# Optimization experiments

Hardware: AMD Instinct MI355X
Metric: run time of the kernel (lower is better)

The kernel has to match this reference:

```python
import jax, jax.numpy as jnp
import numpy as np

DIM = 192
HEADS = 6
HEAD_DIM = DIM // HEADS
K = 3          # kernel_size
PAD = 1
STRIDE = 2
SCALE = HEAD_DIM ** -0.5
B, H, W = 16, 56, 56


def setup_inputs() -> dict:
    key = jax.random.key(0)
    ks = jax.random.split(key, 6)
    x = jax.random.normal(ks[0], (B, H, W, DIM), jnp.float32)
    # Linear weights stored as [in, out] so y = x @ W + b (== torch x @ W.T)
    Wv = jax.random.normal(ks[1], (DIM, DIM), jnp.float32) * 0.05          # v_pj, no bias
    Wa = jax.random.normal(ks[2], (DIM, K**4 * HEADS), jnp.float32) * 0.05  # attn linear
    ba = jax.random.normal(ks[3], (K**4 * HEADS,), jnp.float32) * 0.01
    Wp = jax.random.normal(ks[4], (DIM, DIM), jnp.float32) * 0.05           # proj
    bp = jax.random.normal(ks[5], (DIM,), jnp.float32) * 0.01
    return {"x": x, "Wv": Wv, "Wa": Wa, "ba": ba, "Wp": Wp, "bp": bp}


def reference(x, Wv, Wa, ba, Wp, bp):
    # Dropout layers act as identity (eval mode).
    Bn, Hn, Wn, C = x.shape
    h = -(-Hn // STRIDE)  # ceil(H/stride) = 28
    w = -(-Wn // STRIDE)
    KK = K * K

    # --- value projection + unfold (im2col over K x K window, stride STRIDE) ---
    v = x @ Wv  # [B,H,W,C]
    vp = jnp.pad(v, ((0, 0), (PAD, PAD), (PAD, PAD), (0, 0)))
    # patches: [B,h,w,K*K,C]; loop is over the fixed 3x3 kernel taps only
    patches = jnp.stack(
        [vp[:, i:i + STRIDE * h:STRIDE, j:j + STRIDE * w:STRIDE, :]
         for i in range(K) for j in range(K)], axis=3)
    patches = patches.reshape(Bn, h * w, KK, HEADS, HEAD_DIM)

    # --- attention weights from avg-pooled map (H divisible by STRIDE here) ---
    pooled = x.reshape(Bn, h, STRIDE, w, STRIDE, C).mean(axis=(2, 4))  # [B,h,w,C]
    a = pooled.reshape(Bn, h * w, C) @ Wa + ba                         # [B,hw,K^4*heads]
    a = a.reshape(Bn, h * w, HEADS, KK, KK) * SCALE
    a = jax.nn.softmax(a, axis=-1)

    # --- windowed attention: [B,hw,heads,K2,K2] x [B,hw,K2,heads,hd] ---
    out = jnp.einsum('bnhpq,bnqhd->bnphd', a, patches)  # [B,hw,K2,heads,hd]
    out = out.reshape(Bn, h, w, KK, C)

    # --- fold (scatter-add of overlapping patches back to HxW) ---
    acc = jnp.zeros((Bn, Hn + 2 * PAD, Wn + 2 * PAD, C), x.dtype)
    idx = 0
    for i in range(K):
        for j in range(K):
            acc = acc.at[:, i:i + STRIDE * h:STRIDE, j:j + STRIDE * w:STRIDE, :].add(out[:, :, :, idx, :])
            idx += 1
    y = acc[:, PAD:PAD + Hn, PAD:PAD + Wn, :]

    return y @ Wp + bp
```

## Files before the change

kernel.cpp:

```cpp
#include <hip/hip_runtime.h>
#include <cstdint>
#include <cstddef>

#define DIMC    192
#define NHEADS  6
#define NATT    486
#define NB      16
#define NH      56
#define NWW     56
#define HPOOL   28
#define WPOOL   28
#define NPIX    784
#define VH      58
#define VW      58
#define MROWS   (NB*NH*NWW)
#define MPOOL   (NB*NPIX)
#define SCALE_A 0.17677669529663687f

using bf16x8 = __attribute__((ext_vector_type(8))) short;
using f32x4  = __attribute__((ext_vector_type(4))) float;

static __device__ __forceinline__ unsigned short f2bf(float f) {
    unsigned int u = __float_as_uint(f);
    unsigned int r = (u + 0x7fffu + ((u >> 16) & 1u)) >> 16;
    return (unsigned short)r;
}
static __device__ __forceinline__ float bf2f(unsigned short u) {
    return __uint_as_float((unsigned int)u << 16);
}

__global__ __launch_bounds__(256)
void prep_kernel(const float* __restrict__ Wv, const float* __restrict__ Wp,
                 const float* __restrict__ Wa,
                 unsigned short* __restrict__ WTv, unsigned short* __restrict__ WTp,
                 unsigned short* __restrict__ WaT, unsigned int* __restrict__ vpu)
{
    int idx = blockIdx.x * 256 + threadIdx.x;
    if (idx < 73728) {
        int sel = idx / 36864;
        int r   = idx - sel * 36864;
        int n   = r / DIMC;
        int k   = r - n * DIMC;
        const float* W = sel ? Wp : Wv;
        unsigned short* WT = sel ? WTp : WTv;
        WT[r] = f2bf(W[k * DIMC + n]);
    } else if (idx < 172032) {
        int r = idx - 73728;
        int n = r / DIMC;
        int k = r - n * DIMC;
        WaT[r] = (n < NATT) ? f2bf(Wa[(size_t)k * NATT + n] * SCALE_A) : (unsigned short)0;
    } else {
        int i2   = idx - 172032;
        int cu   = i2 % 96;
        int rest = i2 / 96;
        int b    = rest / 228;
        int p    = rest - b * 228;
        int hi, wi;
        if (p < 58)       { hi = 0;  wi = p; }
        else if (p < 116) { hi = 57; wi = p - 58; }
        else { int q = p - 116; hi = 1 + (q >> 1); wi = (q & 1) * 57; }
        vpu[(((size_t)b * VH + hi) * VW + wi) * 96 + cu] = 0u;
    }
}

static __device__ __forceinline__
void gemm0_body(const float* __restrict__ x, const unsigned short* __restrict__ WT,
                unsigned short* __restrict__ vp, int by, int t, char* smem)
{
    unsigned short* As = (unsigned short*)smem;

    const int l  = t & 63;
    const int w  = t >> 6;
    const int wr = w >> 1;
    const int wc = w & 1;

    const float* Ab = x + (size_t)by * 128 * DIMC;
#pragma unroll
    for (int i = 0; i < 12; ++i) {
        int f = i * 2048 + t * 4;
        float4 v = *(const float4*)(Ab + f);
        int row = f / DIMC;
        int k   = f - row * DIMC;
        ushort4 u;
        u.x = f2bf(v.x); u.y = f2bf(v.y); u.z = f2bf(v.z); u.w = f2bf(v.w);
        int off = (row * 384 + k * 2) ^ ((row & 7) << 4);
        *(ushort4*)((char*)As + off) = u;
    }
    __syncthreads();

    f32x4 acc[2][6];
#pragma unroll
    for (int mi = 0; mi < 2; ++mi)
#pragma unroll
        for (int ni = 0; ni < 6; ++ni) acc[mi][ni] = (f32x4)0.f;

    const int arow0 = wr * 32 + (l & 15);
    const int kb    = (l >> 4) << 4;

#pragma unroll
    for (int ks = 0; ks < 6; ++ks) {
        bf16x8 a[2], b[6];
#pragma unroll
        for (int mi = 0; mi < 2; ++mi) {
            int row = arow0 + mi * 16;
            int off = (row * 384 + ks * 64 + kb) ^ ((row & 7) << 4);
            a[mi] = *(const bf16x8*)((const char*)As + off);
        }
#pragma unroll
        for (int ni = 0; ni < 6; ++ni) {
            int n = wc * 96 + ni * 16 + (l & 15);
            b[ni] = *(const bf16x8*)(WT + (size_t)n * DIMC + ks * 32 + ((l >> 4) << 3));
        }
#pragma unroll
        for (int mi = 0; mi < 2; ++mi)
#pragma unroll
            for (int ni = 0; ni < 6; ++ni)
                acc[mi][ni] = __builtin_amdgcn_mfma_f32_16x16x32_bf16(
                    a[mi], b[ni], acc[mi][ni], 0, 0, 0);
    }

    __syncthreads();
#pragma unroll
    for (int mi = 0; mi < 2; ++mi) {
#pragma unroll
        for (int r = 0; r < 4; ++r) {
            int row = wr * 32 + mi * 16 + ((l >> 4) << 2) + r;
#pragma unroll
            for (int ni = 0; ni < 6; ++ni) {
                int col = wc * 96 + ni * 16 + (l & 15);
                As[row * DIMC + col] = f2bf(acc[mi][ni][r]);
            }
        }
    }
    __syncthreads();
#pragma unroll
    for (int i = 0; i < 6; ++i) {
        int f   = i * 4096 + t * 8;
        int row = f / DIMC;
        int k   = f - row * DIMC;
        int m   = by * 128 + row;
        int bb  = m / (NH * NWW);
        int rr  = m - bb * (NH * NWW);
        int hi  = rr / NWW;
        int wi  = rr - hi * NWW;
        bf16x8 v = *(const bf16x8*)&As[f];
        unsigned short* dst = vp + (((size_t)bb * VH + hi + 1) * VW + (wi + 1)) * DIMC + k;
        *(bf16x8*)dst = v;
    }
}

static __device__ __forceinline__
void pool_body(const float* __restrict__ x, const unsigned short* __restrict__ WaT,
               const float* __restrict__ ba, unsigned short* __restrict__ attn,
               int by, int t, char* smem)
{
    unsigned short* As = (unsigned short*)smem;
    float (*Cs)[489]   = (float(*)[489])smem;
    float* ba_s        = (float*)(smem + 31296);

    const int l  = t & 63;
    const int w  = t >> 6;
    const int wr = w >> 2;
    const int wc = w & 3;

    if (t < NATT) ba_s[t] = ba[t] * SCALE_A;

#pragma unroll
    for (int i = 0; i < 6; ++i) {
        int f   = i * 2048 + t * 4;
        int row = f / DIMC;
        int k   = f - row * DIMC;
        int m   = by * 64 + row;
        int b   = m / NPIX;
        int r   = m - b * NPIX;
        int hh  = r / WPOOL;
        int ww  = r - hh * WPOOL;
        const float* xp = x + (((size_t)(b * NH + hh * 2)) * NWW + ww * 2) * DIMC + k;
        float4 v0 = *(const float4*)(xp);
        float4 v1 = *(const float4*)(xp + DIMC);
        float4 v2 = *(const float4*)(xp + (size_t)NWW * DIMC);
        float4 v3 = *(const float4*)(xp + (size_t)NWW * DIMC + DIMC);
        ushort4 u;
        u.x = f2bf(0.25f * (v0.x + v1.x + v2.x + v3.x));
        u.y = f2bf(0.25f * (v0.y + v1.y + v2.y + v3.y));
        u.z = f2bf(0.25f * (v0.z + v1.z + v2.z + v3.z));
        u.w = f2bf(0.25f * (v0.w + v1.w + v2.w + v3.w));
        int off = (row * 384 + k * 2) ^ ((row & 7) << 4);
        *(ushort4*)((char*)As + off) = u;
    }
    __syncthreads();

    f32x4 acc[2][8];
#pragma unroll
    for (int mi = 0; mi < 2; ++mi)
#pragma unroll
        for (int ni = 0; ni < 8; ++ni) acc[mi][ni] = (f32x4)0.f;

    const int arow0 = wr * 32 + (l & 15);
    const int kb    = (l >> 4) << 4;

#pragma unroll
    for (int ks = 0; ks < 6; ++ks) {
        bf16x8 a[2], b[8];
#pragma unroll
        for (int mi = 0; mi < 2; ++mi) {
            int row = arow0 + mi * 16;
            int off = (row * 384 + ks * 64 + kb) ^ ((row & 7) << 4);
            a[mi] = *(const bf16x8*)((const char*)As + off);
        }
#pragma unroll
        for (int ni = 0; ni < 8; ++ni) {
            int n = wc * 128 + ni * 16 + (l & 15);
            b[ni] = *(const bf16x8*)(WaT + (size_t)n * DIMC + ks * 32 + ((l >> 4) << 3));
        }
#pragma unroll
        for (int mi = 0; mi < 2; ++mi)
#pragma unroll
            for (int ni = 0; ni < 8; ++ni)
                acc[mi][ni] = __builtin_amdgcn_mfma_f32_16x16x32_bf16(
                    a[mi], b[ni], acc[mi][ni], 0, 0, 0);
    }

    __syncthreads();

#pragma unroll
    for (int r0 = 0; r0 < 64; r0 += 16) {
        const int mi = (r0 >> 4) & 1;
        if (wr == (r0 >> 5)) {
#pragma unroll
            for (int ni = 0; ni < 8; ++ni) {
                int col = wc * 128 + ni * 16 + (l & 15);
                if (col < NATT) {
#pragma unroll
                    for (int r = 0; r < 4; ++r)
                        Cs[((l >> 4) << 2) + r][col] =
                            (mi == 0 ? acc[0][ni][r] : acc[1][ni][r]) + ba_s[col];
                }
            }
        }
        __syncthreads();
        for (int g = t; g < 864; g += 512) {
            int lr = g / 54;
            int cg = g - lr * 54;
            const float* ap = &Cs[lr][cg * 9];
            float mx = ap[0];
#pragma unroll
            for (int q = 1; q < 9; ++q) mx = fmaxf(mx, ap[q]);
            float e[9];
            float sum = 0.f;
#pragma unroll
            for (int q = 0; q < 9; ++q) { e[q] = __expf(ap[q] - mx); sum += e[q]; }
            float inv = 1.f / sum;
            int m = by * 64 + r0 + lr;
            unsigned short* dst = attn + ((size_t)m * 54 + cg) * 16;
#pragma unroll
            for (int q = 0; q < 9; ++q) dst[q] = f2bf(e[q] * inv);
        }
        __syncthreads();
    }
}

__global__ __launch_bounds__(512)
void phase1_kernel(const float* __restrict__ x, const unsigned short* __restrict__ WTv,
                   const unsigned short* __restrict__ WaT, const float* __restrict__ ba,
                   unsigned short* __restrict__ vp, unsigned short* __restrict__ attn)
{
    __shared__ __align__(16) char smem[49152];
    const int t = threadIdx.x;
    if (blockIdx.x < 392) gemm0_body(x, WTv, vp, blockIdx.x, t, smem);
    else                  pool_body(x, WaT, ba, attn, blockIdx.x - 392, t, smem);
}

__global__ __launch_bounds__(512)
void gemm1_kernel(const unsigned short* __restrict__ Av, const unsigned short* __restrict__ WT,
                  const float* __restrict__ bias, float* __restrict__ Cv)
{
    __shared__ unsigned short As[128 * DIMC];

    const int t  = threadIdx.x;
    const int l  = t & 63;
    const int w  = t >> 6;
    const int wr = w >> 1;
    const int wc = w & 1;
    const int by = blockIdx.x;

    const unsigned short* Ab = Av + (size_t)by * 128 * DIMC;
#pragma unroll
    for (int i = 0; i < 6; ++i) {
        int f = i * 4096 + t * 8;
        bf16x8 v = *(const bf16x8*)(Ab + f);
        int row = f / DIMC;
        int k   = f - row * DIMC;
        int off = (row * 384 + k * 2) ^ ((row & 7) << 4);
        *(bf16x8*)((char*)As + off) = v;
    }
    __syncthreads();

    f32x4 acc[2][6];
#pragma unroll
    for (int mi = 0; mi < 2; ++mi)
#pragma unroll
        for (int ni = 0; ni < 6; ++ni) acc[mi][ni] = (f32x4)0.f;

    const int arow0 = wr * 32 + (l & 15);
    const int kb    = (l >> 4) << 4;

#pragma unroll
    for (int ks = 0; ks < 6; ++ks) {
        bf16x8 a[2], b[6];
#pragma unroll
        for (int mi = 0; mi < 2; ++mi) {
            int row = arow0 + mi * 16;
            int off = (row * 384 + ks * 64 + kb) ^ ((row & 7) << 4);
            a[mi] = *(const bf16x8*)((const char*)As + off);
        }
#pragma unroll
        for (int ni = 0; ni < 6; ++ni) {
            int n = wc * 96 + ni * 16 + (l & 15);
            b[ni] = *(const bf16x8*)(WT + (size_t)n * DIMC + ks * 32 + ((l >> 4) << 3));
        }
#pragma unroll
        for (int mi = 0; mi < 2; ++mi)
#pragma unroll
            for (int ni = 0; ni < 6; ++ni)
                acc[mi][ni] = __builtin_amdgcn_mfma_f32_16x16x32_bf16(
                    a[mi], b[ni], acc[mi][ni], 0, 0, 0);
    }

    float* fAs = (float*)As;
#pragma unroll
    for (int chunk = 0; chunk < 4; ++chunk) {
        __syncthreads();
        if (wr == chunk) {
#pragma unroll
            for (int mi = 0; mi < 2; ++mi) {
#pragma unroll
                for (int r = 0; r < 4; ++r) {
                    int rowl = mi * 16 + ((l >> 4) << 2) + r;
#pragma unroll
                    for (int ni = 0; ni < 6; ++ni) {
                        int col = wc * 96 + ni * 16 + (l & 15);
                        fAs[rowl * DIMC + col] = acc[mi][ni][r];
                    }
                }
            }
        }
        __syncthreads();
#pragma unroll
        for (int i = 0; i < 3; ++i) {
            int f   = i * 2048 + t * 4;
            int row = f / DIMC;
            int k   = f - row * DIMC;
            int m   = by * 128 + chunk * 32 + row;
            float4 v  = *(const float4*)&fAs[f];
            float4 bv = *(const float4*)&bias[k];
            v.x += bv.x; v.y += bv.y; v.z += bv.z; v.w += bv.w;
            *(float4*)(Cv + (size_t)m * DIMC + k) = v;
        }
    }
}

template<int NI, int NJ>
static __device__ __forceinline__ void gather_body(
    int b, int p, int qc, int head, int c,
    const unsigned short* __restrict__ attn, const unsigned short* __restrict__ vp,
    unsigned short* __restrict__ y)
{
    const int pr = p >> 1;
    const int qr = qc >> 1;

    bf16x8        aw8[NI * NJ];
    unsigned short aw9[NI * NJ];
    ushort2       v[NI * NJ][9];
    bool          ok[NI * NJ];

#pragma unroll
    for (int wi = 0; wi < NI; ++wi) {
        const bool hv  = (NI == 1) || (wi == 0) || (pr + 1 < HPOOL);
        const int  hhs = hv ? (pr + wi) : (HPOOL - 1);
        const int  iof = (NI == 1) ? 1 : (wi ? 0 : 2);
#pragma unroll
        for (int wj = 0; wj < NJ; ++wj) {
            const bool wv  = (NJ == 1) || (wj == 0) || (qr + 1 < WPOOL);
            const int  wws = wv ? (qr + wj) : (WPOOL - 1);
            const int  jof = (NJ == 1) ? 1 : (wj ? 0 : 2);
            const int  idx = wi * NJ + wj;
            ok[idx] = hv && wv;

            const unsigned short* ap = attn +
                ((size_t)((b * NPIX + hhs * WPOOL + wws) * 54 + head * 9 + iof * 3 + jof)) * 16;
            aw8[idx] = *(const bf16x8*)ap;
            aw9[idx] = ap[8];

            const unsigned short* vb = vp +
                (((size_t)(b * VH + 2 * hhs)) * VW + 2 * wws) * DIMC + c;
#pragma unroll
            for (int qi = 0; qi < 3; ++qi)
#pragma unroll
                for (int qj = 0; qj < 3; ++qj)
                    v[idx][qi * 3 + qj] = *(const ushort2*)(vb + ((size_t)qi * VW + qj) * DIMC);
        }
    }

    float accx = 0.f, accy = 0.f;
#pragma unroll
    for (int idx = 0; idx < NI * NJ; ++idx) {
#pragma unroll
        for (int k = 0; k < 9; ++k) {
            float a = ok[idx]
                ? ((k < 8) ? bf2f((unsigned short)aw8[idx][k]) : bf2f(aw9[idx]))
                : 0.f;
            accx = fmaf(a, bf2f(v[idx][k].x), accx);
            accy = fmaf(a, bf2f(v[idx][k].y), accy);
        }
    }

    size_t pix = (size_t)b * (NH * NWW) + (size_t)p * NWW + qc;
    ushort2 r;
    r.x = f2bf(accx);
    r.y = f2bf(accy);
    *(ushort2*)(y + pix * DIMC + c) = r;
}

__global__ __launch_bounds__(192)
void gather_kernel(const unsigned short* __restrict__ attn,
                   const unsigned short* __restrict__ vp,
                   unsigned short* __restrict__ y)
{
    const int t    = threadIdx.x;
    const int pl   = t / 96;
    const int c2   = t - pl * 96;
    const int c    = c2 * 2;
    const int head = c2 >> 4;

    const int flat = blockIdx.x;
    const int wgid = (flat & 7) * 3136 + (flat >> 3);
    const int b    = wgid / 1568;
    const int rr   = wgid - b * 1568;
    const int p    = rr / 28;
    const int wq   = rr - p * 28;
    const int qc   = wq + pl * 28;

    if (p & 1) {
        if (wq & 1) gather_body<2, 2>(b, p, qc, head, c, attn, vp, y);
        else        gather_body<2, 1>(b, p, qc, head, c, attn, vp, y);
    } else {
        if (wq & 1) gather_body<1, 2>(b, p, qc, head, c, attn, vp, y);
        else        gather_body<1, 1>(b, p, qc, head, c, attn, vp, y);
    }
}

extern "C" void kernel_launch(void* const* d_in, const int* in_sizes, int n_in,
                              void* d_out, int out_size, void* d_ws, size_t ws_size,
                              hipStream_t stream)
{
    const float* x  = (const float*)d_in[0];
    const float* Wv = (const float*)d_in[1];
    const float* Wa = (const float*)d_in[2];
    const float* ba = (const float*)d_in[3];
    const float* Wp = (const float*)d_in[4];
    const float* bp = (const float*)d_in[5];
    float* out = (float*)d_out;

    const size_t vp_elems   = (size_t)NB * VH * VW * DIMC;
    const size_t attn_elems = (size_t)MPOOL * 54 * 16;
    const size_t y_elems    = (size_t)MROWS * DIMC;

    unsigned short* vp   = (unsigned short*)d_ws;
    unsigned short* attn = vp + vp_elems;
    unsigned short* y    = attn + attn_elems;
    unsigned short* WTv  = y + y_elems;
    unsigned short* WTp  = WTv + 36864;
    unsigned short* WaT  = WTp + 36864;

    prep_kernel<<<2040, 256, 0, stream>>>(Wv, Wp, Wa, WTv, WTp, WaT, (unsigned int*)vp);

    phase1_kernel<<<588, 512, 0, stream>>>(x, WTv, WaT, ba, vp, attn);

    gather_kernel<<<25088, 192, 0, stream>>>(attn, vp, y);

    gemm1_kernel<<<MROWS / 128, 512, 0, stream>>>(y, WTp, bp, out);
}
```

Baseline: 114.1 us.

## Split phase1 into separate kernels, async LDS staging, vectorized attn stores

```diff
diff --git a/kernel.cpp b/kernel.cpp
--- a/kernel.cpp
+++ b/kernel.cpp
@@ -27,6 +27,12 @@
 }
 static __device__ __forceinline__ float bf2f(unsigned short u) {
     return __uint_as_float((unsigned int)u << 16);
+}
+
+static __device__ __forceinline__ void gload_lds16(const void* src, void* lds) {
+    __builtin_amdgcn_global_load_lds(
+        (const __attribute__((address_space(1))) void*)src,
+        (__attribute__((address_space(3))) void*)lds, 16, 0, 0);
 }
 
 __global__ __launch_bounds__(256)
@@ -63,16 +69,18 @@
     }
 }
 
-static __device__ __forceinline__
-void gemm0_body(const float* __restrict__ x, const unsigned short* __restrict__ WT,
-                unsigned short* __restrict__ vp, int by, int t, char* smem)
-{
-    unsigned short* As = (unsigned short*)smem;
-
+__global__ __launch_bounds__(512)
+void gemm0_kernel(const float* __restrict__ x, const unsigned short* __restrict__ WT,
+                  unsigned short* __restrict__ vp)
+{
+    __shared__ unsigned short As[128 * DIMC];
+
+    const int t  = threadIdx.x;
     const int l  = t & 63;
     const int w  = t >> 6;
     const int wr = w >> 1;
     const int wc = w & 1;
+    const int by = blockIdx.x;
 
     const float* Ab = x + (size_t)by * 128 * DIMC;
 #pragma unroll
@@ -149,19 +157,22 @@
     }
 }
 
-static __device__ __forceinline__
-void pool_body(const float* __restrict__ x, const unsigned short* __restrict__ WaT,
-               const float* __restrict__ ba, unsigned short* __restrict__ attn,
-               int by, int t, char* smem)
-{
+__global__ __launch_bounds__(512)
+void pool_attn_kernel(const float* __restrict__ x, const unsigned short* __restrict__ WaT,
+                      const float* __restrict__ ba, unsigned short* __restrict__ attn)
+{
+    __shared__ __align__(16) char smem[33240];
+
     unsigned short* As = (unsigned short*)smem;
     float (*Cs)[489]   = (float(*)[489])smem;
     float* ba_s        = (float*)(smem + 31296);
 
+    const int t  = threadIdx.x;
     const int l  = t & 63;
     const int w  = t >> 6;
     const int wr = w >> 2;
     const int wc = w & 3;
+    const int by = blockIdx.x;
 
     if (t < NATT) ba_s[t] = ba[t] * SCALE_A;
 
@@ -253,29 +264,35 @@
             float inv = 1.f / sum;
             int m = by * 64 + r0 + lr;
             unsigned short* dst = attn + ((size_t)m * 54 + cg) * 16;
-#pragma unroll
-            for (int q = 0; q < 9; ++q) dst[q] = f2bf(e[q] * inv);
+            bf16x8 ov;
+#pragma unroll
+            for (int q = 0; q < 8; ++q) ov[q] = (short)f2bf(e[q] * inv);
+            *(bf16x8*)dst = ov;
+            dst[8] = f2bf(e[8] * inv);
         }
         __syncthreads();
     }
 }
 
-__global__ __launch_bounds__(512)
-void phase1_kernel(const float* __restrict__ x, const unsigned short* __restrict__ WTv,
-                   const unsigned short* __restrict__ WaT, const float* __restrict__ ba,
-                   unsigned short* __restrict__ vp, unsigned short* __restrict__ attn)
-{
-    __shared__ __align__(16) char smem[49152];
-    const int t = threadIdx.x;
-    if (blockIdx.x < 392) gemm0_body(x, WTv, vp, blockIdx.x, t, smem);
-    else                  pool_body(x, WaT, ba, attn, blockIdx.x - 392, t, smem);
+static __device__ __forceinline__
+void stage_tile_async(const unsigned short* __restrict__ Ab, unsigned short* As, int t)
+{
+#pragma unroll
+    for (int i = 0; i < 6; ++i) {
+        int L     = i * 8192 + t * 16;
+        int row   = L / 384;
+        int inrow = L - row * 384;
+        int s     = (row & 7) << 4;
+        const unsigned short* src = Ab + (size_t)row * DIMC + ((inrow ^ s) >> 1);
+        gload_lds16(src, (char*)As + i * 8192 + (t >> 6) * 1024);
+    }
 }
 
 __global__ __launch_bounds__(512)
 void gemm1_kernel(const unsigned short* __restrict__ Av, const unsigned short* __restrict__ WT,
                   const float* __restrict__ bias, float* __restrict__ Cv)
 {
-    __shared__ unsigned short As[128 * DIMC];
+    __shared__ __align__(16) unsigned short As[128 * DIMC];
 
     const int t  = threadIdx.x;
     const int l  = t & 63;
@@ -284,16 +301,7 @@
     const int wc = w & 1;
     const int by = blockIdx.x;
 
-    const unsigned short* Ab = Av + (size_t)by * 128 * DIMC;
-#pragma unroll
-    for (int i = 0; i < 6; ++i) {
-        int f = i * 4096 + t * 8;
-        bf16x8 v = *(const bf16x8*)(Ab + f);
-        int row = f / DIMC;
-        int k   = f - row * DIMC;
-        int off = (row * 384 + k * 2) ^ ((row & 7) << 4);
-        *(bf16x8*)((char*)As + off) = v;
-    }
+    stage_tile_async(Av + (size_t)by * 128 * DIMC, As, t);
     __syncthreads();
 
     f32x4 acc[2][6];
@@ -475,7 +483,8 @@
 
     prep_kernel<<<2040, 256, 0, stream>>>(Wv, Wp, Wa, WTv, WTp, WaT, (unsigned int*)vp);
 
-    phase1_kernel<<<588, 512, 0, stream>>>(x, WTv, WaT, ba, vp, attn);
+    gemm0_kernel<<<MROWS / 128, 512, 0, stream>>>(x, WTv, vp);
+    pool_attn_kernel<<<MPOOL / 64, 512, 0, stream>>>(x, WaT, ba, attn);
 
     gather_kernel<<<25088, 192, 0, stream>>>(attn, vp, y);
 
```

Measured after the change: 116.4 us. Within noise of the previous version (+2.0%).
